# Optimization experiments

Hardware: AMD Instinct MI355X
Metric: run time of the kernel (lower is better)

## Reference

```python
import jax, jax.numpy as jnp
import numpy as np

B, S, D = 2, 1024, 2048
L = 4
HQ, HKV, HD = 32, 8, 64
I = 5632
V = 32000
EPS = 1e-5
THETA = 10000.0
SCALE = HD ** -0.5
GROUP = HQ // HKV


def setup_inputs() -> dict:
    key = jax.random.key(0)
    ks = jax.random.split(key, 8)
    s = 0.02
    return {
        "input_ids": jax.random.randint(ks[0], (B, S), 0, V, dtype=jnp.int32),
        "positions": jnp.broadcast_to(jnp.arange(S, dtype=jnp.int32), (B, S)),
        "embed": jax.random.normal(ks[1], (V, D), jnp.float32) * s,
        "w_qkv": jax.random.normal(ks[2], (L, D, (HQ + 2 * HKV) * HD), jnp.float32) * s,
        "w_o": jax.random.normal(ks[3], (L, HQ * HD, D), jnp.float32) * s,
        "w_gate_up": jax.random.normal(ks[4], (L, D, 2 * I), jnp.float32) * s,
        "w_down": jax.random.normal(ks[5], (L, I, D), jnp.float32) * s,
        "ln1_w": jnp.ones((L, D), jnp.float32),
        "ln2_w": jnp.ones((L, D), jnp.float32),
        "norm_w": jnp.ones((D,), jnp.float32),
    }


def rmsnorm(x, w):
    var = jnp.mean(x * x, axis=-1, keepdims=True)
    return x * jax.lax.rsqrt(var + EPS) * w


def rope(positions, x):
    # x: [B, S, H, HD]; neox-style rotate-half RoPE
    inv_freq = 1.0 / (THETA ** (jnp.arange(0, HD, 2, dtype=jnp.float32) / HD))
    ang = positions.astype(jnp.float32)[..., None] * inv_freq  # [B, S, HD/2]
    cos = jnp.cos(ang)[:, :, None, :]
    sin = jnp.sin(ang)[:, :, None, :]
    x1, x2 = jnp.split(x, 2, axis=-1)
    return jnp.concatenate([x1 * cos - x2 * sin, x2 * cos + x1 * sin], axis=-1)


def llama_forward(input_ids, positions, embed, w_qkv, w_o, w_gate_up, w_down,
                  ln1_w, ln2_w, norm_w):
    h = embed[input_ids]                      # [B, S, D]
    res = jnp.zeros_like(h)
    causal = jnp.tril(jnp.ones((S, S), dtype=bool))
    neg = jnp.asarray(jnp.finfo(h.dtype).min, h.dtype)

    def layer(carry, params):
        h, res = carry
        wqkv, wo, wgu, wd, l1, l2 = params
        # fused RMSNorm + residual-add (vllm RMSNorm(x, residual) semantics)
        res = h + res
        h = rmsnorm(res, l1)
        # QKV projection + RoPE
        qkv = h @ wqkv
        q, k, v = jnp.split(qkv, [HQ * HD, (HQ + HKV) * HD], axis=-1)
        q = q.reshape(B, S, HQ, HD)
        k = k.reshape(B, S, HKV, HD)
        v = v.reshape(B, S, HKV, HD)
        q = rope(positions, q)
        k = rope(positions, k)
        # GQA: broadcast kv heads across query groups
        k = jnp.repeat(k, GROUP, axis=2)      # [B, S, HQ, HD]
        v = jnp.repeat(v, GROUP, axis=2)
        scores = jnp.einsum('bqhd,bkhd->bhqk', q, k) * SCALE
        scores = jnp.where(causal, scores, neg)
        attn = jax.nn.softmax(scores, axis=-1)
        o = jnp.einsum('bhqk,bkhd->bqhd', attn, v).reshape(B, S, HQ * HD)
        h = o @ wo
        # post-attention fused RMSNorm + residual
        res = h + res
        h = rmsnorm(res, l2)
        # SwiGLU MLP
        gu = h @ wgu
        g, u = jnp.split(gu, 2, axis=-1)
        h = (jax.nn.silu(g) * u) @ wd
        return (h, res), None

    (h, res), _ = jax.lax.scan(layer, (h, res),
                               (w_qkv, w_o, w_gate_up, w_down, ln1_w, ln2_w))
    return rmsnorm(h + res, norm_w)


def reference(input_ids, positions, embed, w_qkv, w_o, w_gate_up, w_down,
              ln1_w, ln2_w, norm_w):
    return llama_forward(input_ids, positions, embed, w_qkv, w_o, w_gate_up,
                         w_down, ln1_w, ln2_w, norm_w)
```

## Files before the change

kernel.cpp:

```cpp
#include <hip/hip_runtime.h>
#include <hip/hip_bf16.h>

#define B_ 2
#define S_ 1024
#define T_ (B_*S_)
#define D_ 2048
#define L_ 4
#define HQ_ 32
#define HKV_ 8
#define HD_ 64
#define I_ 5632
#define EPS_ 1e-5f
#define SCALE_ 0.125f

typedef __attribute__((ext_vector_type(4))) float  float4v;
typedef __attribute__((ext_vector_type(8))) short  short8v;

#define GLOAD16(g, l) \
  __builtin_amdgcn_global_load_lds((const __attribute__((address_space(1))) void*)(g), \
                                   (__attribute__((address_space(3))) void*)(l), 16, 0, 0)

__device__ __forceinline__ short f2bf(float f) {
  union { float f; unsigned u; } c; c.f = f;
  unsigned u = c.u + 0x7fffu + ((c.u >> 16) & 1u);
  return (short)(u >> 16);
}

__device__ __forceinline__ void xcd_swizzle(int gx, int gy, int& bx, int& by) {
  int nwg = gx * gy;
  int orig = by * gx + bx;
  int q = nwg >> 3, r = nwg & 7;
  int xcd = orig & 7, loc = orig >> 3;
  int swz = (xcd < r ? xcd * (q + 1) : r * (q + 1) + (xcd - r) * q) + loc;
  bx = swz / gy;
  by = swz - bx * gy;
}

__global__ __launch_bounds__(256)
void transpose_bf16(const float* __restrict__ in, short* __restrict__ out,
                    int K, int N) {
  __shared__ float t[64][65];
  const int bx = blockIdx.x * 64;
  const int by = blockIdx.y * 64;
  const int tid = threadIdx.x;
  const int lr = tid >> 4;
  const int lc = (tid & 15) * 4;
  #pragma unroll
  for (int j = 0; j < 64; j += 16) {
    float4v v = *(const float4v*)(in + (size_t)(by + lr + j) * N + bx + lc);
    t[lr + j][lc] = v[0]; t[lr + j][lc + 1] = v[1];
    t[lr + j][lc + 2] = v[2]; t[lr + j][lc + 3] = v[3];
  }
  __syncthreads();
  const int nr = tid >> 3;
  const int kc = (tid & 7) * 8;
  #pragma unroll
  for (int j = 0; j < 64; j += 32) {
    short8v y;
    #pragma unroll
    for (int e = 0; e < 8; e++) y[e] = f2bf(t[kc + e][nr + j]);
    *(short8v*)(out + (size_t)(bx + nr + j) * K + by + kc) = y;
  }
}

__global__ __launch_bounds__(256)
void embed_gather(const int* __restrict__ ids, const float* __restrict__ embed,
                  float* __restrict__ h) {
  size_t i = (size_t)blockIdx.x * 256 + threadIdx.x;
  int t  = (int)(i >> 9);
  int d4 = (int)(i & 511);
  ((float4v*)h)[i] = ((const float4v*)(embed + (size_t)ids[t] * D_))[d4];
}

__global__ __launch_bounds__(256)
void rmsnorm_add(const float* __restrict__ x, float* __restrict__ res,
                 const float* __restrict__ w, void* __restrict__ outp,
                 int first, int bf16out) {
  const int row = blockIdx.x;
  const int tid = threadIdx.x;
  const size_t base = (size_t)row * D_;
  float4v v0 = ((const float4v*)(x + base))[tid * 2];
  float4v v1 = ((const float4v*)(x + base))[tid * 2 + 1];
  if (!first) {
    v0 += ((const float4v*)(res + base))[tid * 2];
    v1 += ((const float4v*)(res + base))[tid * 2 + 1];
  }
  ((float4v*)(res + base))[tid * 2]     = v0;
  ((float4v*)(res + base))[tid * 2 + 1] = v1;
  float ss = v0[0]*v0[0] + v0[1]*v0[1] + v0[2]*v0[2] + v0[3]*v0[3]
           + v1[0]*v1[0] + v1[1]*v1[1] + v1[2]*v1[2] + v1[3]*v1[3];
  #pragma unroll
  for (int off = 32; off > 0; off >>= 1) ss += __shfl_xor(ss, off, 64);
  __shared__ float red[4];
  if ((tid & 63) == 0) red[tid >> 6] = ss;
  __syncthreads();
  float tot = red[0] + red[1] + red[2] + red[3];
  float rs = rsqrtf(tot * (1.0f / D_) + EPS_);
  float4v w0 = ((const float4v*)w)[tid * 2];
  float4v w1 = ((const float4v*)w)[tid * 2 + 1];
  float4v o0 = v0 * rs * w0;
  float4v o1 = v1 * rs * w1;
  if (bf16out) {
    short8v y;
    #pragma unroll
    for (int k = 0; k < 4; k++) { y[k] = f2bf(o0[k]); y[k + 4] = f2bf(o1[k]); }
    ((short8v*)((char*)outp + base * 2))[tid] = y;
  } else {
    float* op = (float*)outp + base;
    ((float4v*)op)[tid * 2]     = o0;
    ((float4v*)op)[tid * 2 + 1] = o1;
  }
}

#define BM 128
#define BN 128
#define BKS 32

__global__ __launch_bounds__(512, 4)
void gemm_big128(const short* __restrict__ A, const short* __restrict__ Bt,
                 float* __restrict__ C, int M, int N, int K) {
  __shared__ short sA[2][128 * 64];
  __shared__ short sB[2][128 * 64];
  int bx = blockIdx.x, by = blockIdx.y;
  xcd_swizzle(gridDim.x, gridDim.y, bx, by);
  const int tid  = threadIdx.x;
  const int lane = tid & 63;
  const int wv   = tid >> 6;
  const int wr   = wv >> 2;
  const int wc   = wv & 3;
  const int row0 = by * 128;
  const int col0 = bx * 128;
  const int fr = lane & 15;
  const int g  = lane >> 4;
  const int NT = K >> 6;

  float4v acc[4][2] = {};

  int rS[2], cS[2];
  #pragma unroll
  for (int k = 0; k < 2; k++) {
    int s = tid + k * 512;
    rS[k] = s >> 3;
    cS[k] = (((s & 7) ^ (rS[k] & 7)) << 3);
  }

#define STAGE128(t, buf) do { \
    int k0_ = (t) << 6; \
    _Pragma("unroll") \
    for (int k_ = 0; k_ < 2; k_++) \
      GLOAD16(A  + (size_t)(row0 + rS[k_]) * K + k0_ + cS[k_], \
              &sA[buf][(tid + k_ * 512) * 8]); \
    _Pragma("unroll") \
    for (int k_ = 0; k_ < 2; k_++) \
      GLOAD16(Bt + (size_t)(col0 + rS[k_]) * K + k0_ + cS[k_], \
              &sB[buf][(tid + k_ * 512) * 8]); \
  } while (0)

  STAGE128(0, 0);

  for (int t = 0; t < NT; t++) {
    const int cur = t & 1;
    if (t + 1 < NT) {
      STAGE128(t + 1, cur ^ 1);
      asm volatile("s_waitcnt vmcnt(4)" ::: "memory");
    } else {
      asm volatile("s_waitcnt vmcnt(0)" ::: "memory");
    }
    __builtin_amdgcn_s_barrier();
    __builtin_amdgcn_sched_barrier(0);

    const short* pA = &sA[cur][(wr * 64) * 64];
    const short* pB = &sB[cur][(wc * 32) * 64];
    #pragma unroll
    for (int ks = 0; ks < 2; ks++) {
      const int fswk = ((((ks << 2) | g) ^ (fr & 7)) << 3);
      short8v bfr[2], afr[4];
      #pragma unroll
      for (int ni = 0; ni < 2; ni++)
        bfr[ni] = *(const short8v*)(pB + (ni * 16 + fr) * 64 + fswk);
      #pragma unroll
      for (int m4 = 0; m4 < 4; m4++)
        afr[m4] = *(const short8v*)(pA + (m4 * 16 + fr) * 64 + fswk);
      __builtin_amdgcn_s_setprio(1);
      #pragma unroll
      for (int m4 = 0; m4 < 4; m4++)
        #pragma unroll
        for (int ni = 0; ni < 2; ni++)
          acc[m4][ni] = __builtin_amdgcn_mfma_f32_16x16x32_bf16(
              afr[m4], bfr[ni], acc[m4][ni], 0, 0, 0);
      __builtin_amdgcn_s_setprio(0);
    }
    asm volatile("" ::: "memory");
    __builtin_amdgcn_s_barrier();
  }

  #pragma unroll
  for (int m4 = 0; m4 < 4; m4++)
    #pragma unroll
    for (int ni = 0; ni < 2; ni++) {
      size_t base = (size_t)(row0 + wr * 64 + m4 * 16 + g * 4) * N
                    + col0 + wc * 32 + ni * 16 + fr;
      #pragma unroll
      for (int r = 0; r < 4; r++)
        C[base + (size_t)r * N] = acc[m4][ni][r];
    }
#undef STAGE128
}

__global__ __launch_bounds__(512, 2)
void gemm_glu_big(const short* __restrict__ A, const short* __restrict__ Bt,
                  short* __restrict__ mlp, int K) {
  __shared__ short sA[2][128 * 64];
  __shared__ short sG[2][128 * 64];
  __shared__ short sU[2][128 * 64];
  int bx = blockIdx.x, by = blockIdx.y;
  xcd_swizzle(gridDim.x, gridDim.y, bx, by);
  const int tid  = threadIdx.x;
  const int lane = tid & 63;
  const int wv   = tid >> 6;
  const int wr   = wv >> 2;
  const int wc   = wv & 3;
  const int row0 = by * 128;
  const int col0 = bx * 128;
  const int fr = lane & 15;
  const int g  = lane >> 4;
  const int NT = K >> 6;

  float4v accg[4][2] = {};
  float4v accu[4][2] = {};

  int rS[2], cS[2];
  #pragma unroll
  for (int k = 0; k < 2; k++) {
    int s = tid + k * 512;
    rS[k] = s >> 3;
    cS[k] = (((s & 7) ^ (rS[k] & 7)) << 3);
  }

#define STAGEGLU(t, buf) do { \
    int k0_ = (t) << 6; \
    _Pragma("unroll") \
    for (int k_ = 0; k_ < 2; k_++) \
      GLOAD16(A  + (size_t)(row0 + rS[k_]) * K + k0_ + cS[k_], \
              &sA[buf][(tid + k_ * 512) * 8]); \
    _Pragma("unroll") \
    for (int k_ = 0; k_ < 2; k_++) \
      GLOAD16(Bt + (size_t)(col0 + rS[k_]) * K + k0_ + cS[k_], \
              &sG[buf][(tid + k_ * 512) * 8]); \
    _Pragma("unroll") \
    for (int k_ = 0; k_ < 2; k_++) \
      GLOAD16(Bt + (size_t)(col0 + I_ + rS[k_]) * K + k0_ + cS[k_], \
              &sU[buf][(tid + k_ * 512) * 8]); \
  } while (0)

  STAGEGLU(0, 0);

  for (int t = 0; t < NT; t++) {
    const int cur = t & 1;
    if (t + 1 < NT) {
      STAGEGLU(t + 1, cur ^ 1);
      asm volatile("s_waitcnt vmcnt(6)" ::: "memory");
    } else {
      asm volatile("s_waitcnt vmcnt(0)" ::: "memory");
    }
    __builtin_amdgcn_s_barrier();
    __builtin_amdgcn_sched_barrier(0);

    const short* pA = &sA[cur][(wr * 64) * 64];
    const short* pG = &sG[cur][(wc * 32) * 64];
    const short* pU = &sU[cur][(wc * 32) * 64];
    #pragma unroll
    for (int ks = 0; ks < 2; ks++) {
      const int fswk = ((((ks << 2) | g) ^ (fr & 7)) << 3);
      short8v bg[2], bu[2], afr[4];
      #pragma unroll
      for (int ni = 0; ni < 2; ni++) {
        bg[ni] = *(const short8v*)(pG + (ni * 16 + fr) * 64 + fswk);
        bu[ni] = *(const short8v*)(pU + (ni * 16 + fr) * 64 + fswk);
      }
      #pragma unroll
      for (int m4 = 0; m4 < 4; m4++)
        afr[m4] = *(const short8v*)(pA + (m4 * 16 + fr) * 64 + fswk);
      __builtin_amdgcn_s_setprio(1);
      #pragma unroll
      for (int m4 = 0; m4 < 4; m4++)
        #pragma unroll
        for (int ni = 0; ni < 2; ni++) {
          accg[m4][ni] = __builtin_amdgcn_mfma_f32_16x16x32_bf16(
              afr[m4], bg[ni], accg[m4][ni], 0, 0, 0);
          accu[m4][ni] = __builtin_amdgcn_mfma_f32_16x16x32_bf16(
              afr[m4], bu[ni], accu[m4][ni], 0, 0, 0);
        }
      __builtin_amdgcn_s_setprio(0);
    }
    asm volatile("" ::: "memory");
    __builtin_amdgcn_s_barrier();
  }

  #pragma unroll
  for (int m4 = 0; m4 < 4; m4++)
    #pragma unroll
    for (int ni = 0; ni < 2; ni++) {
      size_t base = (size_t)(row0 + wr * 64 + m4 * 16 + g * 4) * I_
                    + col0 + wc * 32 + ni * 16 + fr;
      #pragma unroll
      for (int r = 0; r < 4; r++) {
        float gv = accg[m4][ni][r], uv = accu[m4][ni][r];
        mlp[base + (size_t)r * I_] = f2bf(gv / (1.0f + __expf(-gv)) * uv);
      }
    }
#undef STAGEGLU
}

__global__ __launch_bounds__(256)
void gemm_qkv_rope(const short* __restrict__ A, const short* __restrict__ Bt,
                   const float* __restrict__ tab, short* __restrict__ qbf,
                   short* __restrict__ kbf, short* __restrict__ vbf, int K) {
  __shared__ short sA[BM * BKS];
  __shared__ short sB[BN * BKS];
  int bx = blockIdx.x, by = blockIdx.y;
  xcd_swizzle(gridDim.x, gridDim.y, bx, by);
  const int tid  = threadIdx.x;
  const int lane = tid & 63;
  const int wave = tid >> 6;
  const int wm = (wave >> 1) << 6;
  const int wn = (wave & 1) << 6;
  const int row0 = by * BM;
  const int col0 = bx * BN;
  const int fr = lane & 15;
  const int fk = (lane >> 4) << 3;
  float4v acc[4][4] = {};

  const int r_st  = tid >> 2;
  const int kc_st = (tid & 3) << 3;
  const short* pA = A  + (size_t)(row0 + r_st) * K + kc_st;
  const short* pB = Bt + (size_t)(col0 + r_st) * K + kc_st;
  const size_t stride64 = (size_t)64 * K;
  short* lA0 = &sA[tid * 8];
  short* lA1 = &sA[(256 + tid) * 8];
  short* lB0 = &sB[tid * 8];
  short* lB1 = &sB[(256 + tid) * 8];

  for (int k0 = 0; k0 < K; k0 += BKS) {
    GLOAD16(pA, lA0);
    GLOAD16(pA + stride64, lA1);
    GLOAD16(pB, lB0);
    GLOAD16(pB + stride64, lB1);
    pA += BKS; pB += BKS;
    __syncthreads();
    short8v af[4], bfr[4];
    #pragma unroll
    for (int f = 0; f < 4; f++) {
      af[f]  = *(const short8v*)(&sA[(wm + f * 16 + fr) * BKS + fk]);
      bfr[f] = *(const short8v*)(&sB[(wn + f * 16 + fr) * BKS + fk]);
    }
    #pragma unroll
    for (int i = 0; i < 4; i++)
      #pragma unroll
      for (int j = 0; j < 4; j++)
        acc[i][j] = __builtin_amdgcn_mfma_f32_16x16x32_bf16(af[i], bfr[j], acc[i][j], 0, 0, 0);
    __syncthreads();
  }
  const int cr = (lane >> 4) << 2;
  const int cc = lane & 15;
  const int head = (col0 + wn) >> 6;

  if (head < HQ_ + HKV_) {
    const float sc = (head < HQ_) ? SCALE_ : 1.0f;
    #pragma unroll
    for (int i = 0; i < 4; i++)
      #pragma unroll
      for (int jj = 0; jj < 2; jj++)
        #pragma unroll
        for (int r = 0; r < 4; r++) {
          int m = row0 + wm + i * 16 + cr + r;
          int b = m >> 10, s = m & (S_ - 1);
          int d1 = jj * 16 + cc;
          float x1 = acc[i][jj][r], x2 = acc[i][jj + 2][r];
          const float* tb = tab + (size_t)m * 64 + d1 * 2;
          float c = tb[0], sn = tb[1];
          short y1 = f2bf((x1 * c - x2 * sn) * sc);
          short y2 = f2bf((x2 * c + x1 * sn) * sc);
          size_t base;
          if (head < HQ_)
            base = ((size_t)((b * HQ_ + head) * S_ + s)) * HD_;
          else
            base = ((size_t)((b * HKV_ + head - HQ_) * S_ + s)) * HD_;
          short* dst = (head < HQ_) ? qbf : kbf;
          dst[base + d1]      = y1;
          dst[base + d1 + 32] = y2;
        }
  } else {
    const int vh = head - HQ_ - HKV_;
    #pragma unroll
    for (int i = 0; i < 4; i++)
      #pragma unroll
      for (int j = 0; j < 4; j++)
        #pragma unroll
        for (int r = 0; r < 4; r++) {
          int m = row0 + wm + i * 16 + cr + r;
          int b = m >> 10, s = m & (S_ - 1);
          vbf[((size_t)((b * HKV_ + vh) * S_ + s)) * HD_ + j * 16 + cc] =
              f2bf(acc[i][j][r]);
        }
  }
}

__global__ __launch_bounds__(256)
void rope_table(const int* __restrict__ pos, float* __restrict__ tab) {
  int i = blockIdx.x * 256 + threadIdx.x;
  int t = i >> 5, ii = i & 31;
  float p = (float)pos[t];
  float freq = __expf(-(float)ii * (9.210340371976184f / 32.0f));
  float ang = p * freq;
  tab[2 * i]     = cosf(ang);
  tab[2 * i + 1] = sinf(ang);
}

#define KPAD 68

__global__ __launch_bounds__(256)
void transpose_v(const short* __restrict__ vbf, short* __restrict__ vtbf) {
  __shared__ short sv[64 * KPAD];
  const int jt = blockIdx.x, kh = blockIdx.y, b = blockIdx.z;
  const int tid = threadIdx.x;
  const short* src = vbf + ((size_t)((b * HKV_ + kh) * S_ + jt * 64)) * HD_;
  #pragma unroll
  for (int it = 0; it < 2; it++) {
    int c = it * 256 + tid;
    int rr = c >> 3, ch = (c & 7) * 8;
    *(short8v*)(&sv[rr * KPAD + ch]) = *(const short8v*)(src + (size_t)rr * HD_ + ch);
  }
  __syncthreads();
  const int dc = tid >> 2;
  const int jc = (tid & 3) * 16;
  short8v o1, o2;
  #pragma unroll
  for (int k = 0; k < 8; k++) o1[k] = sv[(jc + k) * KPAD + dc];
  #pragma unroll
  for (int k = 0; k < 8; k++) o2[k] = sv[(jc + 8 + k) * KPAD + dc];
  short* od = vtbf + ((size_t)((b * HKV_ + kh) * HD_ + dc)) * S_ + jt * 64 + jc;
  *(short8v*)od       = o1;
  *(short8v*)(od + 8) = o2;
}

__global__ __launch_bounds__(256)
void attn_mfma(const short* __restrict__ qbf, const short* __restrict__ kbf,
               const short* __restrict__ vtbf, short* __restrict__ obf) {
  __shared__ short sK[64 * KPAD];
  __shared__ short sVt[64 * KPAD];
  __shared__ short sP[4][16 * KPAD];
  const int qb = blockIdx.x;
  const int h  = blockIdx.y;
  const int b  = blockIdx.z;
  const int kh = h >> 2;
  const int tid  = threadIdx.x;
  const int lane = tid & 63;
  const int wv   = tid >> 6;
  const int q0 = qb * 64;
  const int cc = lane & 15;
  const int g  = lane >> 4;

  short8v qf0, qf1;
  {
    const short* qrow = qbf + ((size_t)((b * HQ_ + h) * S_ + q0 + wv * 16 + cc)) * HD_;
    qf0 = *(const short8v*)(qrow + g * 8);
    qf1 = *(const short8v*)(qrow + g * 8 + 32);
  }
  float4v accO[4] = {};
  float m_r[4], l_r[4];
  #pragma unroll
  for (int r = 0; r < 4; r++) { m_r[r] = -1e30f; l_r[r] = 0.f; }

  const short* kb = kbf  + ((size_t)(b * HKV_ + kh)) * S_ * HD_;
  const short* vb = vtbf + ((size_t)(b * HKV_ + kh)) * HD_ * S_;

  for (int jt = 0; jt <= qb; jt++) {
    const int j0 = jt * 64;
    #pragma unroll
    for (int it = 0; it < 2; it++) {
      int idx = it * 256 + tid;
      int rr = idx >> 3, ch = (idx & 7) * 8;
      *(short8v*)(&sK[rr * KPAD + ch])  = *(const short8v*)(kb + (size_t)(j0 + rr) * HD_ + ch);
      *(short8v*)(&sVt[rr * KPAD + ch]) = *(const short8v*)(vb + (size_t)rr * S_ + j0 + ch);
    }
    __syncthreads();

    float4v sc[4] = {};
    #pragma unroll
    for (int ct = 0; ct < 4; ct++) {
      short8v k0 = *(const short8v*)(&sK[(ct * 16 + cc) * KPAD + g * 8]);
      short8v k1 = *(const short8v*)(&sK[(ct * 16 + cc) * KPAD + g * 8 + 32]);
      sc[ct] = __builtin_amdgcn_mfma_f32_16x16x32_bf16(qf0, k0, sc[ct], 0, 0, 0);
      sc[ct] = __builtin_amdgcn_mfma_f32_16x16x32_bf16(qf1, k1, sc[ct], 0, 0, 0);
    }
    if (jt == qb) {
      #pragma unroll
      for (int ct = 0; ct < 4; ct++)
        #pragma unroll
        for (int r = 0; r < 4; r++)
          if (j0 + ct * 16 + cc > q0 + wv * 16 + g * 4 + r) sc[ct][r] = -1e30f;
    }
    float corr[4];
    #pragma unroll
    for (int r = 0; r < 4; r++) {
      float pm = fmaxf(fmaxf(sc[0][r], sc[1][r]), fmaxf(sc[2][r], sc[3][r]));
      pm = fmaxf(pm, __shfl_xor(pm, 1, 64));
      pm = fmaxf(pm, __shfl_xor(pm, 2, 64));
      pm = fmaxf(pm, __shfl_xor(pm, 4, 64));
      pm = fmaxf(pm, __shfl_xor(pm, 8, 64));
      float mn = fmaxf(m_r[r], pm);
      corr[r] = __expf(m_r[r] - mn);
      m_r[r] = mn;
      float rs = 0.f;
      #pragma unroll
      for (int ct = 0; ct < 4; ct++) {
        float p = __expf(sc[ct][r] - mn);
        sc[ct][r] = p;
        rs += p;
      }
      rs += __shfl_xor(rs, 1, 64);
      rs += __shfl_xor(rs, 2, 64);
      rs += __shfl_xor(rs, 4, 64);
      rs += __shfl_xor(rs, 8, 64);
      l_r[r] = l_r[r] * corr[r] + rs;
    }
    #pragma unroll
    for (int ct = 0; ct < 4; ct++)
      #pragma unroll
      for (int r = 0; r < 4; r++)
        sP[wv][(g * 4 + r) * KPAD + ct * 16 + cc] = f2bf(sc[ct][r]);
    #pragma unroll
    for (int dt = 0; dt < 4; dt++)
      #pragma unroll
      for (int r = 0; r < 4; r++)
        accO[dt][r] *= corr[r];
    short8v pf0 = *(const short8v*)(&sP[wv][cc * KPAD + g * 8]);
    short8v pf1 = *(const short8v*)(&sP[wv][cc * KPAD + g * 8 + 32]);
    #pragma unroll
    for (int dt = 0; dt < 4; dt++) {
      short8v v0 = *(const short8v*)(&sVt[(dt * 16 + cc) * KPAD + g * 8]);
      short8v v1 = *(const short8v*)(&sVt[(dt * 16 + cc) * KPAD + g * 8 + 32]);
      accO[dt] = __builtin_amdgcn_mfma_f32_16x16x32_bf16(pf0, v0, accO[dt], 0, 0, 0);
      accO[dt] = __builtin_amdgcn_mfma_f32_16x16x32_bf16(pf1, v1, accO[dt], 0, 0, 0);
    }
    __syncthreads();
  }
  #pragma unroll
  for (int dt = 0; dt < 4; dt++)
    #pragma unroll
    for (int r = 0; r < 4; r++) {
      int q = q0 + wv * 16 + g * 4 + r;
      obf[((size_t)(b * S_ + q)) * 2048 + h * 64 + dt * 16 + cc] = f2bf(accO[dt][r] / l_r[r]);
    }
}

extern "C" void kernel_launch(void* const* d_in, const int* in_sizes, int n_in,
                              void* d_out, int out_size, void* d_ws, size_t ws_size,
                              hipStream_t stream) {
  const int*   ids   = (const int*)d_in[0];
  const int*   pos   = (const int*)d_in[1];
  const float* embed = (const float*)d_in[2];
  const float* w_qkv = (const float*)d_in[3];
  const float* w_o   = (const float*)d_in[4];
  const float* w_gu  = (const float*)d_in[5];
  const float* w_dn  = (const float*)d_in[6];
  const float* ln1   = (const float*)d_in[7];
  const float* ln2   = (const float*)d_in[8];
  const float* normw = (const float*)d_in[9];
  float* out = (float*)d_out;

  char* p = (char*)d_ws;
  short* wT    = (short*)p; p += (size_t)11264 * 2048 * 2;
  float* h     = (float*)p; p += (size_t)T_ * D_ * 4;
  float* res   = (float*)p; p += (size_t)T_ * D_ * 4;
  short* hnbf  = (short*)p; p += (size_t)T_ * D_ * 2;
  short* obf   = (short*)p; p += (size_t)T_ * D_ * 2;
  short* mlpbf = (short*)p; p += (size_t)T_ * I_ * 2;
  float* tab   = (float*)p; p += (size_t)T_ * 64 * 4;
  short* qbf   = (short*)p; p += (size_t)B_ * HQ_ * S_ * HD_ * 2;
  short* kbf   = (short*)p; p += (size_t)B_ * HKV_ * S_ * HD_ * 2;
  short* vbf   = (short*)p; p += (size_t)B_ * HKV_ * S_ * HD_ * 2;
  short* vtbf  = (short*)p; p += (size_t)B_ * HKV_ * HD_ * S_ * 2;

  embed_gather<<<T_ * D_ / 4 / 256, 256, 0, stream>>>(ids, embed, h);
  rope_table<<<T_ * 32 / 256, 256, 0, stream>>>(pos, tab);

  for (int l = 0; l < L_; l++) {
    rmsnorm_add<<<T_, 256, 0, stream>>>(h, res, ln1 + l * D_, hnbf, l == 0 ? 1 : 0, 1);

    transpose_bf16<<<dim3(3072 / 64, 2048 / 64), 256, 0, stream>>>(
        w_qkv + (size_t)l * 2048 * 3072, wT, 2048, 3072);
    gemm_qkv_rope<<<dim3(3072 / BN, T_ / BM), 256, 0, stream>>>(
        hnbf, wT, tab, qbf, kbf, vbf, 2048);

    transpose_v<<<dim3(16, 8, 2), 256, 0, stream>>>(vbf, vtbf);
    attn_mfma<<<dim3(16, 32, 2), 256, 0, stream>>>(qbf, kbf, vtbf, obf);

    transpose_bf16<<<dim3(2048 / 64, 2048 / 64), 256, 0, stream>>>(
        w_o + (size_t)l * 2048 * 2048, wT, 2048, 2048);
    gemm_big128<<<dim3(2048 / 128, T_ / 128), 512, 0, stream>>>(
        obf, wT, h, T_, 2048, 2048);

    rmsnorm_add<<<T_, 256, 0, stream>>>(h, res, ln2 + l * D_, hnbf, 0, 1);

    transpose_bf16<<<dim3(11264 / 64, 2048 / 64), 256, 0, stream>>>(
        w_gu + (size_t)l * 2048 * 11264, wT, 2048, 11264);
    gemm_glu_big<<<dim3(I_ / 128, T_ / 128), 512, 0, stream>>>(
        hnbf, wT, mlpbf, 2048);

    transpose_bf16<<<dim3(2048 / 64, 5632 / 64), 256, 0, stream>>>(
        w_dn + (size_t)l * 5632 * 2048, wT, 5632, 2048);
    gemm_big128<<<dim3(2048 / 128, T_ / 128), 512, 0, stream>>>(
        mlpbf, wT, h, T_, 2048, 5632);
  }
  rmsnorm_add<<<T_, 256, 0, stream>>>(h, res, normw, out, 0, 0);
}
```

Before: 1.828 ms.

## Rewrite QKV+RoPE GEMM with double-buffered swizzled LDS and 512-thread blocks

Replaces the single-buffered 256-thread QKV GEMM (BK=32, a sync before and after each tile) with a 512-thread kernel. It uses BK=64 tiles double-buffered in LDS with an XOR swizzle, prefetches the next tile before waiting on the current one, and raises MFMA priority with setprio. Each wave now computes a 32x64 sub-tile. The RoPE and head-scatter epilogue is kept but adapted to the new fragment layout. The aim is to overlap global loads with MFMA work and cut LDS bank conflicts, at the cost of more LDS per block.

```diff
diff --git a/kernel.cpp b/kernel.cpp
--- a/kernel.cpp
+++ b/kernel.cpp
@@ -111,10 +111,6 @@
     ((float4v*)op)[tid * 2 + 1] = o1;
   }
 }
-
-#define BM 128
-#define BN 128
-#define BKS 32
 
 __global__ __launch_bounds__(512, 4)
 void gemm_big128(const short* __restrict__ A, const short* __restrict__ Bt,
@@ -312,98 +308,122 @@
 #undef STAGEGLU
 }
 
-__global__ __launch_bounds__(256)
-void gemm_qkv_rope(const short* __restrict__ A, const short* __restrict__ Bt,
-                   const float* __restrict__ tab, short* __restrict__ qbf,
-                   short* __restrict__ kbf, short* __restrict__ vbf, int K) {
-  __shared__ short sA[BM * BKS];
-  __shared__ short sB[BN * BKS];
+__global__ __launch_bounds__(512, 4)
+void gemm_qkv_big(const short* __restrict__ A, const short* __restrict__ Bt,
+                  const float* __restrict__ tab, short* __restrict__ qbf,
+                  short* __restrict__ kbf, short* __restrict__ vbf, int K) {
+  __shared__ short sA[2][128 * 64];
+  __shared__ short sB[2][128 * 64];
   int bx = blockIdx.x, by = blockIdx.y;
   xcd_swizzle(gridDim.x, gridDim.y, bx, by);
   const int tid  = threadIdx.x;
   const int lane = tid & 63;
-  const int wave = tid >> 6;
-  const int wm = (wave >> 1) << 6;
-  const int wn = (wave & 1) << 6;
-  const int row0 = by * BM;
-  const int col0 = bx * BN;
+  const int wv   = tid >> 6;
+  const int wm   = (wv >> 1) * 32;
+  const int wn   = (wv & 1) * 64;
+  const int row0 = by * 128;
+  const int col0 = bx * 128;
   const int fr = lane & 15;
-  const int fk = (lane >> 4) << 3;
-  float4v acc[4][4] = {};
-
-  const int r_st  = tid >> 2;
-  const int kc_st = (tid & 3) << 3;
-  const short* pA = A  + (size_t)(row0 + r_st) * K + kc_st;
-  const short* pB = Bt + (size_t)(col0 + r_st) * K + kc_st;
-  const size_t stride64 = (size_t)64 * K;
-  short* lA0 = &sA[tid * 8];
-  short* lA1 = &sA[(256 + tid) * 8];
-  short* lB0 = &sB[tid * 8];
-  short* lB1 = &sB[(256 + tid) * 8];
-
-  for (int k0 = 0; k0 < K; k0 += BKS) {
-    GLOAD16(pA, lA0);
-    GLOAD16(pA + stride64, lA1);
-    GLOAD16(pB, lB0);
-    GLOAD16(pB + stride64, lB1);
-    pA += BKS; pB += BKS;
-    __syncthreads();
-    short8v af[4], bfr[4];
-    #pragma unroll
-    for (int f = 0; f < 4; f++) {
-      af[f]  = *(const short8v*)(&sA[(wm + f * 16 + fr) * BKS + fk]);
-      bfr[f] = *(const short8v*)(&sB[(wn + f * 16 + fr) * BKS + fk]);
-    }
-    #pragma unroll
-    for (int i = 0; i < 4; i++)
-      #pragma unroll
-      for (int j = 0; j < 4; j++)
-        acc[i][j] = __builtin_amdgcn_mfma_f32_16x16x32_bf16(af[i], bfr[j], acc[i][j], 0, 0, 0);
-    __syncthreads();
-  }
-  const int cr = (lane >> 4) << 2;
-  const int cc = lane & 15;
+  const int g  = lane >> 4;
+  const int NT = K >> 6;
+
+  float4v acc[2][4] = {};
+
+  int rS[2], cS[2];
+  #pragma unroll
+  for (int k = 0; k < 2; k++) {
+    int s = tid + k * 512;
+    rS[k] = s >> 3;
+    cS[k] = (((s & 7) ^ (rS[k] & 7)) << 3);
+  }
+
+#define STAGEQKV(t, buf) do { \
+    int k0_ = (t) << 6; \
+    _Pragma("unroll") \
+    for (int k_ = 0; k_ < 2; k_++) \
+      GLOAD16(A  + (size_t)(row0 + rS[k_]) * K + k0_ + cS[k_], \
+              &sA[buf][(tid + k_ * 512) * 8]); \
+    _Pragma("unroll") \
+    for (int k_ = 0; k_ < 2; k_++) \
+      GLOAD16(Bt + (size_t)(col0 + rS[k_]) * K + k0_ + cS[k_], \
+              &sB[buf][(tid + k_ * 512) * 8]); \
+  } while (0)
+
+  STAGEQKV(0, 0);
+
+  for (int t = 0; t < NT; t++) {
+    const int cur = t & 1;
+    if (t + 1 < NT) {
+      STAGEQKV(t + 1, cur ^ 1);
+      asm volatile("s_waitcnt vmcnt(4)" ::: "memory");
+    } else {
+      asm volatile("s_waitcnt vmcnt(0)" ::: "memory");
+    }
+    __builtin_amdgcn_s_barrier();
+    __builtin_amdgcn_sched_barrier(0);
+
+    const short* pA = &sA[cur][wm * 64];
+    const short* pB = &sB[cur][wn * 64];
+    #pragma unroll
+    for (int ks = 0; ks < 2; ks++) {
+      const int fswk = ((((ks << 2) | g) ^ (fr & 7)) << 3);
+      short8v afr[2], bfr[4];
+      #pragma unroll
+      for (int m2 = 0; m2 < 2; m2++)
+        afr[m2] = *(const short8v*)(pA + (m2 * 16 + fr) * 64 + fswk);
+      #pragma unroll
+      for (int ni = 0; ni < 4; ni++)
+        bfr[ni] = *(const short8v*)(pB + (ni * 16 + fr) * 64 + fswk);
+      __builtin_amdgcn_s_setprio(1);
+      #pragma unroll
+      for (int m2 = 0; m2 < 2; m2++)
+        #pragma unroll
+        for (int ni = 0; ni < 4; ni++)
+          acc[m2][ni] = __builtin_amdgcn_mfma_f32_16x16x32_bf16(
+              afr[m2], bfr[ni], acc[m2][ni], 0, 0, 0);
+      __builtin_amdgcn_s_setprio(0);
+    }
+    asm volatile("" ::: "memory");
+    __builtin_amdgcn_s_barrier();
+  }
+
   const int head = (col0 + wn) >> 6;
-
   if (head < HQ_ + HKV_) {
     const float sc = (head < HQ_) ? SCALE_ : 1.0f;
-    #pragma unroll
-    for (int i = 0; i < 4; i++)
+    short* dst = (head < HQ_) ? qbf : kbf;
+    const int hh = (head < HQ_) ? head : head - HQ_;
+    const int HN = (head < HQ_) ? HQ_ : HKV_;
+    #pragma unroll
+    for (int m2 = 0; m2 < 2; m2++)
       #pragma unroll
       for (int jj = 0; jj < 2; jj++)
         #pragma unroll
         for (int r = 0; r < 4; r++) {
-          int m = row0 + wm + i * 16 + cr + r;
+          int m = row0 + wm + m2 * 16 + g * 4 + r;
           int b = m >> 10, s = m & (S_ - 1);
-          int d1 = jj * 16 + cc;
-          float x1 = acc[i][jj][r], x2 = acc[i][jj + 2][r];
+          int d1 = jj * 16 + fr;
+          float x1 = acc[m2][jj][r], x2 = acc[m2][jj + 2][r];
           const float* tb = tab + (size_t)m * 64 + d1 * 2;
           float c = tb[0], sn = tb[1];
-          short y1 = f2bf((x1 * c - x2 * sn) * sc);
-          short y2 = f2bf((x2 * c + x1 * sn) * sc);
-          size_t base;
-          if (head < HQ_)
-            base = ((size_t)((b * HQ_ + head) * S_ + s)) * HD_;
-          else
-            base = ((size_t)((b * HKV_ + head - HQ_) * S_ + s)) * HD_;
-          short* dst = (head < HQ_) ? qbf : kbf;
-          dst[base + d1]      = y1;
-          dst[base + d1 + 32] = y2;
+          size_t base = ((size_t)((b * HN + hh) * S_ + s)) * HD_;
+          dst[base + d1]      = f2bf((x1 * c - x2 * sn) * sc);
+          dst[base + d1 + 32] = f2bf((x2 * c + x1 * sn) * sc);
         }
   } else {
     const int vh = head - HQ_ - HKV_;
     #pragma unroll
-    for (int i = 0; i < 4; i++)
-      #pragma unroll
-      for (int j = 0; j < 4; j++)
+    for (int m2 = 0; m2 < 2; m2++)
+      #pragma unroll
+      for (int ni = 0; ni < 4; ni++)
         #pragma unroll
         for (int r = 0; r < 4; r++) {
-          int m = row0 + wm + i * 16 + cr + r;
+          int m = row0 + wm + m2 * 16 + g * 4 + r;
           int b = m >> 10, s = m & (S_ - 1);
-          vbf[((size_t)((b * HKV_ + vh) * S_ + s)) * HD_ + j * 16 + cc] =
-              f2bf(acc[i][j][r]);
+          vbf[((size_t)((b * HKV_ + vh) * S_ + s)) * HD_ + ni * 16 + fr] =
+              f2bf(acc[m2][ni][r]);
         }
   }
+#undef STAGEQKV
 }
 
 __global__ __launch_bounds__(256)
@@ -591,7 +611,7 @@
 
     transpose_bf16<<<dim3(3072 / 64, 2048 / 64), 256, 0, stream>>>(
         w_qkv + (size_t)l * 2048 * 3072, wT, 2048, 3072);
-    gemm_qkv_rope<<<dim3(3072 / BN, T_ / BM), 256, 0, stream>>>(
+    gemm_qkv_big<<<dim3(3072 / 128, T_ / 128), 512, 0, stream>>>(
         hnbf, wT, tab, qbf, kbf, vbf, 2048);
 
     transpose_v<<<dim3(16, 8, 2), 256, 0, stream>>>(vbf, vtbf);
```

Result: faster. 1.766 ms (-3.4%).
